# Kernel tuning notes

Hardware: AMD Instinct MI355X
Metric: run time of the kernel (lower is better)

Reference implementation:

```python
import jax, jax.numpy as jnp
import numpy as np

N_NODES = 100000
N_EDGES = 1600000
N_GRAPHS = 128
BEHAVIOR_DIM = 32
LLM_DIM = 768
LLM_PROJ = 32
HIDDEN = 64
NUM_CLASSES = 2
INPUT_DIM = 64 + 16 + LLM_PROJ + BEHAVIOR_DIM  # 144


def gcn_conv(h, edge_index, edge_weight, W, b, n):
    """PyG GCNConv: linear -> gcn_norm with self-loops -> scatter-add at target."""
    h = h @ W  # [N, out]
    row, col = edge_index[0], edge_index[1]
    loop = jnp.arange(n)
    row_f = jnp.concatenate([row, loop])
    col_f = jnp.concatenate([col, loop])
    ew_f = jnp.concatenate([edge_weight, jnp.ones((n,), h.dtype)])
    deg = jax.ops.segment_sum(ew_f, col_f, num_segments=n)
    dinv = jnp.where(deg > 0, jax.lax.rsqrt(deg), 0.0)
    norm = dinv[row_f] * ew_f * dinv[col_f]  # [E+N]
    out = jax.ops.segment_sum(norm[:, None] * h[row_f], col_f, num_segments=n)
    return out + b


def global_mean_pool(x, batch, num_graphs):
    s = jax.ops.segment_sum(x, batch, num_segments=num_graphs)
    cnt = jax.ops.segment_sum(jnp.ones((x.shape[0],), x.dtype), batch, num_segments=num_graphs)
    return s / jnp.maximum(cnt, 1.0)[:, None]


def setup_inputs() -> dict:
    key = jax.random.key(0)
    ks = jax.random.split(key, 16)
    inp = {
        "x_names": jax.random.randint(ks[0], (N_NODES,), 0, 20000),
        "x_types": jax.random.randint(ks[1], (N_NODES,), 0, 100),
        "x_behaviors": jax.random.normal(ks[2], (N_NODES, BEHAVIOR_DIM), jnp.float32),
        "edge_index": jax.random.randint(ks[3], (2, N_EDGES), 0, N_NODES),
        "edge_weight": jax.random.uniform(ks[4], (N_EDGES,), jnp.float32),
        "batch": jnp.sort(jax.random.randint(ks[5], (N_NODES,), 0, N_GRAPHS)),
        "llm_features": jax.random.normal(ks[6], (N_NODES, LLM_DIM), jnp.float32),
        # parameters
        "name_emb": jax.random.normal(ks[7], (20000, 64), jnp.float32),
        "type_emb": jax.random.normal(ks[8], (100, 16), jnp.float32),
        "llm_proj_w": jax.random.normal(ks[9], (LLM_DIM, LLM_PROJ), jnp.float32) * 0.02,
        "llm_proj_b": jnp.zeros((LLM_PROJ,), jnp.float32),
        "conv1_w": jax.random.normal(ks[10], (INPUT_DIM, HIDDEN), jnp.float32) * 0.08,
        "conv1_b": jnp.zeros((HIDDEN,), jnp.float32),
        "conv2_w": jax.random.normal(ks[11], (HIDDEN, HIDDEN), jnp.float32) * 0.12,
        "conv2_b": jnp.zeros((HIDDEN,), jnp.float32),
        "cls_w": jax.random.normal(ks[12], (HIDDEN, NUM_CLASSES), jnp.float32) * 0.12,
        "cls_b": jnp.zeros((NUM_CLASSES,), jnp.float32),
    }
    return inp


def reference(x_names, x_types, x_behaviors, edge_index, edge_weight, batch,
              llm_features, name_emb, type_emb, llm_proj_w, llm_proj_b,
              conv1_w, conv1_b, conv2_w, conv2_b, cls_w, cls_b):
    n = x_names.shape[0]
    name_feat = name_emb[x_names]          # [N, 64]
    type_feat = type_emb[x_types]          # [N, 16]
    llm_feat = llm_features @ llm_proj_w + llm_proj_b  # [N, 32]
    x = jnp.concatenate([name_feat, type_feat, llm_feat, x_behaviors], axis=1)
    # dropout is identity in eval mode
    x = jax.nn.relu(gcn_conv(x, edge_index, edge_weight, conv1_w, conv1_b, n))
    x = jax.nn.relu(gcn_conv(x, edge_index, edge_weight, conv2_w, conv2_b, n))
    x = global_mean_pool(x, batch, N_GRAPHS)  # [G, HIDDEN]
    return x @ cls_w + cls_b                   # [G, 2]
```

## Files before the change

kernel.cpp:

```cpp
#include <hip/hip_runtime.h>
#include <cstdint>
#include <cstddef>

typedef __attribute__((ext_vector_type(8))) _Float16 f16x8;
typedef __attribute__((ext_vector_type(4))) _Float16 f16x4;
typedef __attribute__((ext_vector_type(4))) float f32x4;

__device__ __forceinline__ f16x8 cvt8(const float4& p, const float4& q) {
  f16x8 r;
  r[0] = (_Float16)p.x; r[1] = (_Float16)p.y; r[2] = (_Float16)p.z; r[3] = (_Float16)p.w;
  r[4] = (_Float16)q.x; r[5] = (_Float16)q.y; r[6] = (_Float16)q.z; r[7] = (_Float16)q.w;
  return r;
}


__global__ void prep_kernel(const float* __restrict__ pw, const float* __restrict__ pb,
                            const float* __restrict__ w1, const float* __restrict__ w2,
                            _Float16* __restrict__ Bf, float* __restrict__ biasf,
                            _Float16* __restrict__ B2f, int* __restrict__ cnt, int n) {
  int idx = blockIdx.x * 256 + threadIdx.x;
  if (idx < n) cnt[idx] = 0;
  if (idx < 896 * 64) {
    int gk = idx >> 6, col = idx & 63;
    float val;
    if (gk < 768) {
      float acc = 0.0f;
      #pragma unroll 8
      for (int m = 0; m < 32; ++m) acc = fmaf(pw[gk * 32 + m], w1[(80 + m) * 64 + col], acc);
      val = acc;
    } else if (gk < 832) val = w1[(gk - 768) * 64 + col];
    else if (gk < 848)   val = w1[(64 + gk - 832) * 64 + col];
    else if (gk < 864)   val = w1[(112 + gk - 848) * 64 + col];
    else if (gk < 880)   val = w1[(128 + gk - 864) * 64 + col];
    else                 val = 0.0f;
    int chunk = gk >> 5, k = gk & 31;
    int g, j;
    if (k < 16) { g = k >> 2; j = k & 3; } else { int k2 = k - 16; g = k2 >> 2; j = 4 + (k2 & 3); }
    Bf[((size_t)(chunk * 4 + g) * 64 + col) * 8 + j] = (_Float16)val;
  } else if (idx < 896 * 64 + 64) {
    int col = idx - 896 * 64;
    float acc = 0.0f;
    for (int m = 0; m < 32; ++m) acc = fmaf(pb[m], w1[(80 + m) * 64 + col], acc);
    biasf[col] = acc;
  } else if (idx < 896 * 64 + 64 + 64 * 64) {
    int q2 = idx - (896 * 64 + 64);
    int gk = q2 >> 6, col = q2 & 63;
    float val = w2[gk * 64 + col];
    int chunk = gk >> 5, k = gk & 31;
    int g = k >> 3, j = k & 7;
    B2f[((size_t)(chunk * 4 + g) * 64 + col) * 8 + j] = (_Float16)val;
  }
}


__global__ void cnt_kernel(const int* __restrict__ ei, int* __restrict__ cnt, int E) {
  int e = blockIdx.x * 256 + threadIdx.x;
  if (e < E) atomicAdd(&cnt[ei[E + e]], 1);
}

__global__ __launch_bounds__(256) void scan_blk(const int* __restrict__ cnt,
                                                int* __restrict__ colp,
                                                int* __restrict__ bsum, int n) {
  __shared__ int ws[4];
  int t = threadIdx.x, lane = t & 63, w = t >> 6;
  int i = blockIdx.x * 256 + t;
  int v = (i < n) ? cnt[i] : 0;
  int x = v;
  #pragma unroll
  for (int off = 1; off < 64; off <<= 1) { int y = __shfl_up(x, off); if (lane >= off) x += y; }
  if (lane == 63) ws[w] = x;
  __syncthreads();
  if (t == 0) {
    int s = 0;
    #pragma unroll
    for (int k = 0; k < 4; ++k) { int tmp = ws[k]; ws[k] = s; s += tmp; }
    bsum[blockIdx.x] = s;
  }
  __syncthreads();
  if (i < n) colp[i] = ws[w] + x - v;
}

__global__ __launch_bounds__(512) void scan_top(int* __restrict__ bsum,
                                                int* __restrict__ colp, int nb, int n) {
  __shared__ int ws[8];
  int t = threadIdx.x, lane = t & 63, w = t >> 6;
  int v = (t < nb) ? bsum[t] : 0;
  int x = v;
  #pragma unroll
  for (int off = 1; off < 64; off <<= 1) { int y = __shfl_up(x, off); if (lane >= off) x += y; }
  if (lane == 63) ws[w] = x;
  __syncthreads();
  if (t == 0) {
    int s = 0;
    #pragma unroll
    for (int k = 0; k < 8; ++k) { int tmp = ws[k]; ws[k] = s; s += tmp; }
  }
  __syncthreads();
  int excl = ws[w] + x - v;
  if (t < nb) bsum[t] = excl;
  if (t == nb - 1) colp[n] = excl + v;
}

__global__ void scan_add(int* __restrict__ colp, const int* __restrict__ bsum, int n) {
  int i = blockIdx.x * 256 + threadIdx.x;
  if (i < n) colp[i] += bsum[blockIdx.x];
}

__global__ void fill_kernel(const int* __restrict__ ei, const float* __restrict__ ew,
                            int* __restrict__ colp, int2* __restrict__ csr, int E) {
  int e = blockIdx.x * 256 + threadIdx.x;
  if (e >= E) return;
  int row = ei[e], col = ei[E + e];
  int pos = atomicAdd(&colp[col], 1);
  csr[pos] = make_int2(row, __float_as_int(ew[e]));
}

__global__ void degsum_kernel(const int* __restrict__ colp, const int2* __restrict__ csr,
                              float* __restrict__ dinv, int n) {
  int j = blockIdx.x * 256 + threadIdx.x;
  if (j >= n) return;
  int e0 = (j > 0) ? colp[j - 1] : 0;
  int e1 = colp[j];
  float s = 1.0f;
  for (int e = e0; e < e1; ++e) s += __int_as_float(csr[e].y);
  dinv[j] = rsqrtf(s);
}


__device__ __forceinline__ void loadBf(const _Float16* __restrict__ Bf, int c, int g, int r16,
                                       f16x8 (&bf)[4]) {
  #pragma unroll
  for (int ct = 0; ct < 4; ++ct)
    bf[ct] = *(const f16x8*)(Bf + ((size_t)(c * 4 + g) * 64 + ct * 16 + r16) * 8);
}

__device__ __forceinline__ void mfma8(f32x4 (&acc)[2][4], const f16x8& a0, const f16x8& a1,
                                      const f16x8 (&bf)[4]) {
  #pragma unroll
  for (int ct = 0; ct < 4; ++ct) {
    acc[0][ct] = __builtin_amdgcn_mfma_f32_16x16x32_f16(a0, bf[ct], acc[0][ct], 0, 0, 0);
    acc[1][ct] = __builtin_amdgcn_mfma_f32_16x16x32_f16(a1, bf[ct], acc[1][ct], 0, 0, 0);
  }
}

__global__ __launch_bounds__(256, 3) void gemm1_kernel(
    const float* __restrict__ llm, const _Float16* __restrict__ Bf,
    const int* __restrict__ names, const int* __restrict__ types,
    const float* __restrict__ beh, const float* __restrict__ nemb,
    const float* __restrict__ temb, const float* __restrict__ biasf,
    const float* __restrict__ dinv, _Float16* __restrict__ out, int n)
{
  int nwg = gridDim.x;
  int b = blockIdx.x;
  int q = nwg >> 3, r = nwg & 7;
  int xcd = b & 7, bidx = b >> 3;
  int swz = (xcd < r ? xcd * (q + 1) : r * (q + 1) + (xcd - r) * q) + bidx;

  int w = swz * 4 + (threadIdx.x >> 6);
  int nw = (n + 31) >> 5;
  if (w >= nw) return;
  int lane = threadIdx.x & 63;
  int g = lane >> 4, r16 = lane & 15;
  int base = w * 32;

  int arow0 = base + r16;      if (arow0 > n - 1) arow0 = n - 1;
  int arow1 = base + 16 + r16; if (arow1 > n - 1) arow1 = n - 1;
  int nm0 = names[arow0], nm1 = names[arow1];
  int tp0 = types[arow0], tp1 = types[arow1];

  const float* pA0 = llm + (size_t)arow0 * 768 + g * 4;
  const float* pA1 = llm + (size_t)arow1 * 768 + g * 4;

  f32x4 acc[2][4];
  #pragma unroll
  for (int i = 0; i < 2; ++i)
    #pragma unroll
    for (int j = 0; j < 4; ++j) { acc[i][j][0] = 0.f; acc[i][j][1] = 0.f; acc[i][j][2] = 0.f; acc[i][j][3] = 0.f; }

  float4 X0l = *(const float4*)(pA0 +  0), X0h = *(const float4*)(pA0 + 16);
  float4 X1l = *(const float4*)(pA1 +  0), X1h = *(const float4*)(pA1 + 16);
  float4 Y0l = *(const float4*)(pA0 + 32), Y0h = *(const float4*)(pA0 + 48);
  float4 Y1l = *(const float4*)(pA1 + 32), Y1h = *(const float4*)(pA1 + 48);
  float4 Z0l = *(const float4*)(pA0 + 64), Z0h = *(const float4*)(pA0 + 80);
  float4 Z1l = *(const float4*)(pA1 + 64), Z1h = *(const float4*)(pA1 + 80);

  f16x8 bf[4], a0, a1;

  #pragma unroll 1
  for (int cc = 0; cc < 7; ++cc) {
    const int c = cc * 3;
    loadBf(Bf, c, g, r16, bf);
    a0 = cvt8(X0l, X0h); a1 = cvt8(X1l, X1h);
    X0l = *(const float4*)(pA0 + (c + 3) * 32);
    X0h = *(const float4*)(pA0 + (c + 3) * 32 + 16);
    X1l = *(const float4*)(pA1 + (c + 3) * 32);
    X1h = *(const float4*)(pA1 + (c + 3) * 32 + 16);
    __builtin_amdgcn_sched_barrier(0);
    mfma8(acc, a0, a1, bf);
    loadBf(Bf, c + 1, g, r16, bf);
    a0 = cvt8(Y0l, Y0h); a1 = cvt8(Y1l, Y1h);
    Y0l = *(const float4*)(pA0 + (c + 4) * 32);
    Y0h = *(const float4*)(pA0 + (c + 4) * 32 + 16);
    Y1l = *(const float4*)(pA1 + (c + 4) * 32);
    Y1h = *(const float4*)(pA1 + (c + 4) * 32 + 16);
    __builtin_amdgcn_sched_barrier(0);
    mfma8(acc, a0, a1, bf);
    loadBf(Bf, c + 2, g, r16, bf);
    a0 = cvt8(Z0l, Z0h); a1 = cvt8(Z1l, Z1h);
    Z0l = *(const float4*)(pA0 + (c + 5) * 32);
    Z0h = *(const float4*)(pA0 + (c + 5) * 32 + 16);
    Z1l = *(const float4*)(pA1 + (c + 5) * 32);
    Z1h = *(const float4*)(pA1 + (c + 5) * 32 + 16);
    __builtin_amdgcn_sched_barrier(0);
    mfma8(acc, a0, a1, bf);
  }

  loadBf(Bf, 21, g, r16, bf);
  a0 = cvt8(X0l, X0h); a1 = cvt8(X1l, X1h);
  mfma8(acc, a0, a1, bf);
  loadBf(Bf, 22, g, r16, bf);
  a0 = cvt8(Y0l, Y0h); a1 = cvt8(Y1l, Y1h);
  mfma8(acc, a0, a1, bf);
  loadBf(Bf, 23, g, r16, bf);
  a0 = cvt8(Z0l, Z0h); a1 = cvt8(Z1l, Z1h);
  mfma8(acc, a0, a1, bf);

  const float* pN0 = nemb + (size_t)nm0 * 64 + g * 4;
  const float* pN1 = nemb + (size_t)nm1 * 64 + g * 4;
  #pragma unroll
  for (int t = 0; t < 2; ++t) {
    float4 l0 = *(const float4*)(pN0 + t * 32), h0 = *(const float4*)(pN0 + t * 32 + 16);
    float4 l1 = *(const float4*)(pN1 + t * 32), h1 = *(const float4*)(pN1 + t * 32 + 16);
    loadBf(Bf, 24 + t, g, r16, bf);
    a0 = cvt8(l0, h0); a1 = cvt8(l1, h1);
    mfma8(acc, a0, a1, bf);
  }
  {
    float4 l0 = *(const float4*)(temb + (size_t)tp0 * 16 + g * 4);
    float4 h0 = *(const float4*)(beh + (size_t)arow0 * 32 + g * 4);
    float4 l1 = *(const float4*)(temb + (size_t)tp1 * 16 + g * 4);
    float4 h1 = *(const float4*)(beh + (size_t)arow1 * 32 + g * 4);
    loadBf(Bf, 26, g, r16, bf);
    a0 = cvt8(l0, h0); a1 = cvt8(l1, h1);
    mfma8(acc, a0, a1, bf);
  }
  {
    const float4 z = make_float4(0.f, 0.f, 0.f, 0.f);
    float4 l0 = *(const float4*)(beh + (size_t)arow0 * 32 + 16 + g * 4);
    float4 l1 = *(const float4*)(beh + (size_t)arow1 * 32 + 16 + g * 4);
    loadBf(Bf, 27, g, r16, bf);
    a0 = cvt8(l0, z); a1 = cvt8(l1, z);
    mfma8(acc, a0, a1, bf);
  }

  float dv0[4], dv1[4];
  #pragma unroll
  for (int rr = 0; rr < 4; ++rr) {
    int n0 = base + g * 4 + rr;      dv0[rr] = dinv[n0 < n ? n0 : n - 1];
    int n1 = base + 16 + g * 4 + rr; dv1[rr] = dinv[n1 < n ? n1 : n - 1];
  }
  #pragma unroll
  for (int ct = 0; ct < 4; ++ct) {
    int col = ct * 16 + r16;
    float bfc = biasf[col];
    #pragma unroll
    for (int rr = 0; rr < 4; ++rr) {
      int node0 = base + g * 4 + rr;
      if (node0 < n) out[(size_t)node0 * 64 + col] = (_Float16)((acc[0][ct][rr] + bfc) * dv0[rr]);
      int node1 = base + 16 + g * 4 + rr;
      if (node1 < n) out[(size_t)node1 * 64 + col] = (_Float16)((acc[1][ct][rr] + bfc) * dv1[rr]);
    }
  }
}


__global__ __launch_bounds__(256, 4) void gemm2_kernel(
    const _Float16* __restrict__ h, const _Float16* __restrict__ B2f,
    const float* __restrict__ dinv, _Float16* __restrict__ out, int n)
{
  int w = blockIdx.x * 4 + (threadIdx.x >> 6);
  int nw = (n + 31) >> 5;
  if (w >= nw) return;
  int lane = threadIdx.x & 63;
  int g = lane >> 4, r16 = lane & 15;
  int base = w * 32;
  int arow0 = base + r16;      if (arow0 > n - 1) arow0 = n - 1;
  int arow1 = base + 16 + r16; if (arow1 > n - 1) arow1 = n - 1;

  f32x4 acc[2][4];
  #pragma unroll
  for (int i = 0; i < 2; ++i)
    #pragma unroll
    for (int j = 0; j < 4; ++j) { acc[i][j][0] = 0.f; acc[i][j][1] = 0.f; acc[i][j][2] = 0.f; acc[i][j][3] = 0.f; }

  #pragma unroll
  for (int c = 0; c < 2; ++c) {
    f16x8 bf[4];
    loadBf(B2f, c, g, r16, bf);
    f16x8 a0 = *(const f16x8*)(h + (size_t)arow0 * 64 + c * 32 + g * 8);
    f16x8 a1 = *(const f16x8*)(h + (size_t)arow1 * 64 + c * 32 + g * 8);
    mfma8(acc, a0, a1, bf);
  }

  float dv0[4], dv1[4];
  #pragma unroll
  for (int rr = 0; rr < 4; ++rr) {
    int n0 = base + g * 4 + rr;      dv0[rr] = dinv[n0 < n ? n0 : n - 1];
    int n1 = base + 16 + g * 4 + rr; dv1[rr] = dinv[n1 < n ? n1 : n - 1];
  }
  #pragma unroll
  for (int ct = 0; ct < 4; ++ct) {
    int col = ct * 16 + r16;
    #pragma unroll
    for (int rr = 0; rr < 4; ++rr) {
      int node0 = base + g * 4 + rr;
      if (node0 < n) out[(size_t)node0 * 64 + col] = (_Float16)(acc[0][ct][rr] * dv0[rr]);
      int node1 = base + 16 + g * 4 + rr;
      if (node1 < n) out[(size_t)node1 * 64 + col] = (_Float16)(acc[1][ct][rr] * dv1[rr]);
    }
  }
}


template <typename OUT>
__global__ __launch_bounds__(256) void agg_kernel(
    const _Float16* __restrict__ hp, const int* __restrict__ colp,
    const int2* __restrict__ csr, const float* __restrict__ dinv,
    const float* __restrict__ bias, OUT* __restrict__ out, int n)
{
  int wid = threadIdx.x >> 6, lane = threadIdx.x & 63;
  int j = blockIdx.x * 4 + wid;
  if (j >= n) return;
  float dj = dinv[j];
  float hj = (float)hp[(size_t)j * 64 + lane];
  int e0 = (j > 0) ? colp[j - 1] : 0;
  int e1 = colp[j];
  float s0 = 0.0f, s1 = 0.0f;
  int e = e0;
  for (; e + 8 <= e1; e += 8) {
    int2 m0 = csr[e],     m1 = csr[e + 1], m2 = csr[e + 2], m3 = csr[e + 3];
    int2 m4 = csr[e + 4], m5 = csr[e + 5], m6 = csr[e + 6], m7 = csr[e + 7];
    float f0 = (float)hp[(size_t)m0.x * 64 + lane];
    float f1 = (float)hp[(size_t)m1.x * 64 + lane];
    float f2 = (float)hp[(size_t)m2.x * 64 + lane];
    float f3 = (float)hp[(size_t)m3.x * 64 + lane];
    float f4 = (float)hp[(size_t)m4.x * 64 + lane];
    float f5 = (float)hp[(size_t)m5.x * 64 + lane];
    float f6 = (float)hp[(size_t)m6.x * 64 + lane];
    float f7 = (float)hp[(size_t)m7.x * 64 + lane];
    s0 = fmaf(__int_as_float(m0.y), f0, s0);
    s1 = fmaf(__int_as_float(m1.y), f1, s1);
    s0 = fmaf(__int_as_float(m2.y), f2, s0);
    s1 = fmaf(__int_as_float(m3.y), f3, s1);
    s0 = fmaf(__int_as_float(m4.y), f4, s0);
    s1 = fmaf(__int_as_float(m5.y), f5, s1);
    s0 = fmaf(__int_as_float(m6.y), f6, s0);
    s1 = fmaf(__int_as_float(m7.y), f7, s1);
  }
  for (; e + 2 <= e1; e += 2) {
    int2 m0 = csr[e], m1 = csr[e + 1];
    float f0 = (float)hp[(size_t)m0.x * 64 + lane];
    float f1 = (float)hp[(size_t)m1.x * 64 + lane];
    s0 = fmaf(__int_as_float(m0.y), f0, s0);
    s1 = fmaf(__int_as_float(m1.y), f1, s1);
  }
  if (e < e1) {
    int2 m = csr[e];
    s0 = fmaf(__int_as_float(m.y), (float)hp[(size_t)m.x * 64 + lane], s0);
  }
  float acc = bias[lane] + dj * (hj + s0 + s1);
  out[(size_t)j * 64 + lane] = (OUT)fmaxf(acc, 0.0f);
}


__global__ __launch_bounds__(256) void pool_kernel(const float* __restrict__ x,
                                                   const int* __restrict__ batch,
                                                   float* __restrict__ pooled, int n) {
  __shared__ float red[4][64];
  __shared__ int range_s[2];
  int gph = blockIdx.x;
  int tid = threadIdx.x, wid = tid >> 6, lane = tid & 63;
  if (tid < 2) {
    int target = gph + tid;
    int lo = 0, hi = n;
    while (lo < hi) { int m = (lo + hi) >> 1; if (batch[m] < target) lo = m + 1; else hi = m; }
    range_s[tid] = lo;
  }
  __syncthreads();
  int lo = range_s[0], hi = range_s[1];
  float acc = 0.0f;
  for (int i = lo + wid; i < hi; i += 4) acc += x[(size_t)i * 64 + lane];
  red[wid][lane] = acc;
  __syncthreads();
  if (tid < 64) {
    float sum = red[0][lane] + red[1][lane] + red[2][lane] + red[3][lane];
    float cntf = (float)(hi - lo);
    pooled[gph * 64 + lane] = sum / fmaxf(cntf, 1.0f);
  }
}

__global__ void cls_kernel(const float* __restrict__ pooled, const float* __restrict__ cw,
                           const float* __restrict__ cb, float* __restrict__ out) {
  int t = threadIdx.x;
  int gph = t >> 1, c = t & 1;
  float acc = cb[c];
  #pragma unroll 8
  for (int k = 0; k < 64; ++k) acc = fmaf(pooled[gph * 64 + k], cw[k * 2 + c], acc);
  out[gph * 2 + c] = acc;
}


extern "C" void kernel_launch(void* const* d_in, const int* in_sizes, int n_in,
                              void* d_out, int out_size, void* d_ws, size_t ws_size,
                              hipStream_t stream) {
  const int*   x_names  = (const int*)  d_in[0];
  const int*   x_types  = (const int*)  d_in[1];
  const float* behav    = (const float*)d_in[2];
  const int*   ei       = (const int*)  d_in[3];
  const float* ew       = (const float*)d_in[4];
  const int*   batch    = (const int*)  d_in[5];
  const float* llm      = (const float*)d_in[6];
  const float* name_emb = (const float*)d_in[7];
  const float* type_emb = (const float*)d_in[8];
  const float* pw       = (const float*)d_in[9];
  const float* pb       = (const float*)d_in[10];
  const float* w1       = (const float*)d_in[11];
  const float* b1       = (const float*)d_in[12];
  const float* w2       = (const float*)d_in[13];
  const float* b2       = (const float*)d_in[14];
  const float* cw       = (const float*)d_in[15];
  const float* cb       = (const float*)d_in[16];

  const int N = in_sizes[0];
  const int E = in_sizes[4];
  const int nb = (N + 255) / 256;
  const int eb = (E + 255) / 256;
  const int gblocks = ((N + 31) / 32 + 3) / 4;

  char* p = (char*)d_ws;
  auto alloc = [&](size_t bytes) -> void* {
    void* r = (void*)p; p += (bytes + 255) & ~(size_t)255; return r;
  };
  float*     dinv   = (float*)    alloc((size_t)N * 4);
  int*       cnt    = (int*)      alloc((size_t)N * 4);
  int*       colp   = (int*)      alloc((size_t)(N + 1) * 4);
  int2*      csr    = (int2*)     alloc((size_t)E * 8);
  int*       bsum   = (int*)      alloc((size_t)(nb + 1) * 4);
  _Float16*  Bf     = (_Float16*) alloc((size_t)896 * 64 * 2);
  _Float16*  B2f    = (_Float16*) alloc((size_t)64 * 64 * 2);
  float*     biasf  = (float*)    alloc((size_t)64 * 4);
  _Float16*  hp1    = (_Float16*) alloc((size_t)N * 64 * 2);
  _Float16*  y1     = (_Float16*) alloc((size_t)N * 64 * 2);
  _Float16*  hp2    = (_Float16*) alloc((size_t)N * 64 * 2);
  float*     y2     = (float*)    alloc((size_t)N * 64 * 4);
  float*     pooled = (float*)    alloc((size_t)128 * 64 * 4);
  (void)ws_size; (void)n_in; (void)out_size;

  int prep_blocks = (896 * 64 + 64 + 64 * 64 + 255) / 256;
  if (prep_blocks < nb) prep_blocks = nb;
  prep_kernel<<<prep_blocks, 256, 0, stream>>>(pw, pb, w1, w2, Bf, biasf, B2f, cnt, N);
  cnt_kernel<<<eb, 256, 0, stream>>>(ei, cnt, E);
  scan_blk<<<nb, 256, 0, stream>>>(cnt, colp, bsum, N);
  scan_top<<<1, 512, 0, stream>>>(bsum, colp, nb, N);
  scan_add<<<nb, 256, 0, stream>>>(colp, bsum, N);
  fill_kernel<<<eb, 256, 0, stream>>>(ei, ew, colp, csr, E);
  degsum_kernel<<<nb, 256, 0, stream>>>(colp, csr, dinv, N);

  gemm1_kernel<<<gblocks, 256, 0, stream>>>(llm, Bf, x_names, x_types, behav,
                                            name_emb, type_emb, biasf, dinv, hp1, N);
  agg_kernel<_Float16><<<(N + 3) / 4, 256, 0, stream>>>(hp1, colp, csr, dinv, b1, y1, N);
  gemm2_kernel<<<gblocks, 256, 0, stream>>>(y1, B2f, dinv, hp2, N);
  agg_kernel<float><<<(N + 3) / 4, 256, 0, stream>>>(hp2, colp, csr, dinv, b2, y2, N);
  pool_kernel<<<128, 256, 0, stream>>>(y2, batch, pooled, N);
  cls_kernel<<<1, 256, 0, stream>>>(pooled, cw, cb, (float*)d_out);
}
```

Baseline: 490.2 us.

## Stage LLM rows in LDS for gemm1 and split output columns across waves

gemm1 now has each 256-thread block load a 32-row tile of the fp32 LLM features with fully coalesced float4 loads, convert it to fp16 into shared memory, and then let four waves share it. Each wave computes 16 rows by 32 columns. Before, each wave streamed its own 32 rows with strided per-lane loads. The B-fragment layout in prep is changed to a simple k>>3 / k&7 packing to match the new A fragment order, and the tail embedding gathers are reworked to match. This is meant to improve global load coalescing and shrink register use, at the cost of about 50KB of LDS per block, a barrier, and less overlap of loads with MFMA.

```diff
diff --git a/kernel.cpp b/kernel.cpp
--- a/kernel.cpp
+++ b/kernel.cpp
@@ -30,12 +30,10 @@
       val = acc;
     } else if (gk < 832) val = w1[(gk - 768) * 64 + col];
     else if (gk < 848)   val = w1[(64 + gk - 832) * 64 + col];
-    else if (gk < 864)   val = w1[(112 + gk - 848) * 64 + col];
-    else if (gk < 880)   val = w1[(128 + gk - 864) * 64 + col];
+    else if (gk < 880)   val = w1[(112 + gk - 848) * 64 + col];
     else                 val = 0.0f;
     int chunk = gk >> 5, k = gk & 31;
-    int g, j;
-    if (k < 16) { g = k >> 2; j = k & 3; } else { int k2 = k - 16; g = k2 >> 2; j = 4 + (k2 & 3); }
+    int g = k >> 3, j = k & 7;
     Bf[((size_t)(chunk * 4 + g) * 64 + col) * 8 + j] = (_Float16)val;
   } else if (idx < 896 * 64 + 64) {
     int col = idx - 896 * 64;
@@ -127,21 +125,8 @@
 }
 
 
-__device__ __forceinline__ void loadBf(const _Float16* __restrict__ Bf, int c, int g, int r16,
-                                       f16x8 (&bf)[4]) {
-  #pragma unroll
-  for (int ct = 0; ct < 4; ++ct)
-    bf[ct] = *(const f16x8*)(Bf + ((size_t)(c * 4 + g) * 64 + ct * 16 + r16) * 8);
-}
-
-__device__ __forceinline__ void mfma8(f32x4 (&acc)[2][4], const f16x8& a0, const f16x8& a1,
-                                      const f16x8 (&bf)[4]) {
-  #pragma unroll
-  for (int ct = 0; ct < 4; ++ct) {
-    acc[0][ct] = __builtin_amdgcn_mfma_f32_16x16x32_f16(a0, bf[ct], acc[0][ct], 0, 0, 0);
-    acc[1][ct] = __builtin_amdgcn_mfma_f32_16x16x32_f16(a1, bf[ct], acc[1][ct], 0, 0, 0);
-  }
-}
+#define G1_ROWS 32
+#define G1_STR  776
 
 __global__ __launch_bounds__(256, 3) void gemm1_kernel(
     const float* __restrict__ llm, const _Float16* __restrict__ Bf,
@@ -150,129 +135,121 @@
     const float* __restrict__ temb, const float* __restrict__ biasf,
     const float* __restrict__ dinv, _Float16* __restrict__ out, int n)
 {
+  __shared__ _Float16 As[G1_ROWS][G1_STR];
+
   int nwg = gridDim.x;
   int b = blockIdx.x;
   int q = nwg >> 3, r = nwg & 7;
   int xcd = b & 7, bidx = b >> 3;
   int swz = (xcd < r ? xcd * (q + 1) : r * (q + 1) + (xcd - r) * q) + bidx;
 
-  int w = swz * 4 + (threadIdx.x >> 6);
-  int nw = (n + 31) >> 5;
-  if (w >= nw) return;
-  int lane = threadIdx.x & 63;
-  int g = lane >> 4, r16 = lane & 15;
-  int base = w * 32;
-
-  int arow0 = base + r16;      if (arow0 > n - 1) arow0 = n - 1;
-  int arow1 = base + 16 + r16; if (arow1 > n - 1) arow1 = n - 1;
-  int nm0 = names[arow0], nm1 = names[arow1];
-  int tp0 = types[arow0], tp1 = types[arow1];
-
-  const float* pA0 = llm + (size_t)arow0 * 768 + g * 4;
-  const float* pA1 = llm + (size_t)arow1 * 768 + g * 4;
-
-  f32x4 acc[2][4];
-  #pragma unroll
-  for (int i = 0; i < 2; ++i)
-    #pragma unroll
-    for (int j = 0; j < 4; ++j) { acc[i][j][0] = 0.f; acc[i][j][1] = 0.f; acc[i][j][2] = 0.f; acc[i][j][3] = 0.f; }
-
-  float4 X0l = *(const float4*)(pA0 +  0), X0h = *(const float4*)(pA0 + 16);
-  float4 X1l = *(const float4*)(pA1 +  0), X1h = *(const float4*)(pA1 + 16);
-  float4 Y0l = *(const float4*)(pA0 + 32), Y0h = *(const float4*)(pA0 + 48);
-  float4 Y1l = *(const float4*)(pA1 + 32), Y1h = *(const float4*)(pA1 + 48);
-  float4 Z0l = *(const float4*)(pA0 + 64), Z0h = *(const float4*)(pA0 + 80);
-  float4 Z1l = *(const float4*)(pA1 + 64), Z1h = *(const float4*)(pA1 + 80);
-
-  f16x8 bf[4], a0, a1;
-
-  #pragma unroll 1
-  for (int cc = 0; cc < 7; ++cc) {
-    const int c = cc * 3;
-    loadBf(Bf, c, g, r16, bf);
-    a0 = cvt8(X0l, X0h); a1 = cvt8(X1l, X1h);
-    X0l = *(const float4*)(pA0 + (c + 3) * 32);
-    X0h = *(const float4*)(pA0 + (c + 3) * 32 + 16);
-    X1l = *(const float4*)(pA1 + (c + 3) * 32);
-    X1h = *(const float4*)(pA1 + (c + 3) * 32 + 16);
-    __builtin_amdgcn_sched_barrier(0);
-    mfma8(acc, a0, a1, bf);
-    loadBf(Bf, c + 1, g, r16, bf);
-    a0 = cvt8(Y0l, Y0h); a1 = cvt8(Y1l, Y1h);
-    Y0l = *(const float4*)(pA0 + (c + 4) * 32);
-    Y0h = *(const float4*)(pA0 + (c + 4) * 32 + 16);
-    Y1l = *(const float4*)(pA1 + (c + 4) * 32);
-    Y1h = *(const float4*)(pA1 + (c + 4) * 32 + 16);
-    __builtin_amdgcn_sched_barrier(0);
-    mfma8(acc, a0, a1, bf);
-    loadBf(Bf, c + 2, g, r16, bf);
-    a0 = cvt8(Z0l, Z0h); a1 = cvt8(Z1l, Z1h);
-    Z0l = *(const float4*)(pA0 + (c + 5) * 32);
-    Z0h = *(const float4*)(pA0 + (c + 5) * 32 + 16);
-    Z1l = *(const float4*)(pA1 + (c + 5) * 32);
-    Z1h = *(const float4*)(pA1 + (c + 5) * 32 + 16);
-    __builtin_amdgcn_sched_barrier(0);
-    mfma8(acc, a0, a1, bf);
-  }
-
-  loadBf(Bf, 21, g, r16, bf);
-  a0 = cvt8(X0l, X0h); a1 = cvt8(X1l, X1h);
-  mfma8(acc, a0, a1, bf);
-  loadBf(Bf, 22, g, r16, bf);
-  a0 = cvt8(Y0l, Y0h); a1 = cvt8(Y1l, Y1h);
-  mfma8(acc, a0, a1, bf);
-  loadBf(Bf, 23, g, r16, bf);
-  a0 = cvt8(Z0l, Z0h); a1 = cvt8(Z1l, Z1h);
-  mfma8(acc, a0, a1, bf);
-
-  const float* pN0 = nemb + (size_t)nm0 * 64 + g * 4;
-  const float* pN1 = nemb + (size_t)nm1 * 64 + g * 4;
-  #pragma unroll
-  for (int t = 0; t < 2; ++t) {
-    float4 l0 = *(const float4*)(pN0 + t * 32), h0 = *(const float4*)(pN0 + t * 32 + 16);
-    float4 l1 = *(const float4*)(pN1 + t * 32), h1 = *(const float4*)(pN1 + t * 32 + 16);
-    loadBf(Bf, 24 + t, g, r16, bf);
-    a0 = cvt8(l0, h0); a1 = cvt8(l1, h1);
-    mfma8(acc, a0, a1, bf);
-  }
+  const int tid = threadIdx.x;
+  const int base = swz * G1_ROWS;
+
+  const float* srcbase = llm + (size_t)base * 768;
+  bool safe = (base + G1_ROWS <= n);
+  #pragma unroll
+  for (int i = 0; i < 24; ++i) {
+    int f = i * 1024 + tid * 4;
+    int row = f / 768;
+    int k = f - row * 768;
+    const float* sp;
+    if (safe) sp = srcbase + f;
+    else {
+      int grow = base + row; if (grow > n - 1) grow = n - 1;
+      sp = llm + (size_t)grow * 768 + k;
+    }
+    float4 v = *(const float4*)sp;
+    f16x4 h;
+    h[0] = (_Float16)v.x; h[1] = (_Float16)v.y;
+    h[2] = (_Float16)v.z; h[3] = (_Float16)v.w;
+    *(f16x4*)&As[row][k] = h;
+  }
+  __syncthreads();
+
+  const int lane = tid & 63, wv = tid >> 6;
+  const int g = lane >> 4, r16 = lane & 15;
+  const int rowHalf = (wv & 1) * 16;
+  const int cbase = (wv >> 1) * 2;
+
+  int arowG = base + rowHalf + r16; if (arowG > n - 1) arowG = n - 1;
+  int nm = names[arowG], tp = types[arowG];
+
+  f32x4 acc0, acc1;
+  acc0[0] = 0.f; acc0[1] = 0.f; acc0[2] = 0.f; acc0[3] = 0.f;
+  acc1 = acc0;
+
+  #pragma unroll 4
+  for (int c = 0; c < 24; ++c) {
+    f16x8 b0 = *(const f16x8*)(Bf + ((size_t)(c * 4 + g) * 64 + cbase * 16 + r16) * 8);
+    f16x8 b1 = *(const f16x8*)(Bf + ((size_t)(c * 4 + g) * 64 + (cbase + 1) * 16 + r16) * 8);
+    f16x8 a = *(const f16x8*)&As[rowHalf + r16][c * 32 + g * 8];
+    acc0 = __builtin_amdgcn_mfma_f32_16x16x32_f16(a, b0, acc0, 0, 0, 0);
+    acc1 = __builtin_amdgcn_mfma_f32_16x16x32_f16(a, b1, acc1, 0, 0, 0);
+  }
+
+  auto tailStep = [&](int c, const float4& p, const float4& qv) {
+    f16x8 b0 = *(const f16x8*)(Bf + ((size_t)(c * 4 + g) * 64 + cbase * 16 + r16) * 8);
+    f16x8 b1 = *(const f16x8*)(Bf + ((size_t)(c * 4 + g) * 64 + (cbase + 1) * 16 + r16) * 8);
+    f16x8 a = cvt8(p, qv);
+    acc0 = __builtin_amdgcn_mfma_f32_16x16x32_f16(a, b0, acc0, 0, 0, 0);
+    acc1 = __builtin_amdgcn_mfma_f32_16x16x32_f16(a, b1, acc1, 0, 0, 0);
+  };
+
   {
-    float4 l0 = *(const float4*)(temb + (size_t)tp0 * 16 + g * 4);
-    float4 h0 = *(const float4*)(beh + (size_t)arow0 * 32 + g * 4);
-    float4 l1 = *(const float4*)(temb + (size_t)tp1 * 16 + g * 4);
-    float4 h1 = *(const float4*)(beh + (size_t)arow1 * 32 + g * 4);
-    loadBf(Bf, 26, g, r16, bf);
-    a0 = cvt8(l0, h0); a1 = cvt8(l1, h1);
-    mfma8(acc, a0, a1, bf);
+    const float* pN = nemb + (size_t)nm * 64 + g * 8;
+    tailStep(24, *(const float4*)pN, *(const float4*)(pN + 4));
+    tailStep(25, *(const float4*)(pN + 32), *(const float4*)(pN + 36));
+  }
+  {
+    const float* q0 = (g < 2) ? (temb + (size_t)tp * 16 + g * 8)
+                              : (beh + (size_t)arowG * 32 + (size_t)(g - 2) * 8);
+    tailStep(26, *(const float4*)q0, *(const float4*)(q0 + 4));
   }
   {
     const float4 z = make_float4(0.f, 0.f, 0.f, 0.f);
-    float4 l0 = *(const float4*)(beh + (size_t)arow0 * 32 + 16 + g * 4);
-    float4 l1 = *(const float4*)(beh + (size_t)arow1 * 32 + 16 + g * 4);
-    loadBf(Bf, 27, g, r16, bf);
-    a0 = cvt8(l0, z); a1 = cvt8(l1, z);
-    mfma8(acc, a0, a1, bf);
-  }
-
-  float dv0[4], dv1[4];
+    const float* q1 = beh + (size_t)arowG * 32 + 16 + (size_t)(g & 1) * 8;
+    float4 p = *(const float4*)q1, qv = *(const float4*)(q1 + 4);
+    if (g >= 2) { p = z; qv = z; }
+    tailStep(27, p, qv);
+  }
+
+  int nodeBase = base + rowHalf + g * 4;
+  float dv[4];
   #pragma unroll
   for (int rr = 0; rr < 4; ++rr) {
-    int n0 = base + g * 4 + rr;      dv0[rr] = dinv[n0 < n ? n0 : n - 1];
-    int n1 = base + 16 + g * 4 + rr; dv1[rr] = dinv[n1 < n ? n1 : n - 1];
-  }
-  #pragma unroll
-  for (int ct = 0; ct < 4; ++ct) {
-    int col = ct * 16 + r16;
+    int nd = nodeBase + rr;
+    dv[rr] = dinv[nd < n ? nd : n - 1];
+  }
+  #pragma unroll
+  for (int ct2 = 0; ct2 < 2; ++ct2) {
+    int col = (cbase + ct2) * 16 + r16;
     float bfc = biasf[col];
+    f32x4 av = (ct2 == 0) ? acc0 : acc1;
     #pragma unroll
     for (int rr = 0; rr < 4; ++rr) {
-      int node0 = base + g * 4 + rr;
-      if (node0 < n) out[(size_t)node0 * 64 + col] = (_Float16)((acc[0][ct][rr] + bfc) * dv0[rr]);
-      int node1 = base + 16 + g * 4 + rr;
-      if (node1 < n) out[(size_t)node1 * 64 + col] = (_Float16)((acc[1][ct][rr] + bfc) * dv1[rr]);
+      int nd = nodeBase + rr;
+      if (nd < n) out[(size_t)nd * 64 + col] = (_Float16)((av[rr] + bfc) * dv[rr]);
     }
   }
 }
 
+
+__device__ __forceinline__ void loadBf(const _Float16* __restrict__ Bf, int c, int g, int r16,
+                                       f16x8 (&bf)[4]) {
+  #pragma unroll
+  for (int ct = 0; ct < 4; ++ct)
+    bf[ct] = *(const f16x8*)(Bf + ((size_t)(c * 4 + g) * 64 + ct * 16 + r16) * 8);
+}
+
+__device__ __forceinline__ void mfma8(f32x4 (&acc)[2][4], const f16x8& a0, const f16x8& a1,
+                                      const f16x8 (&bf)[4]) {
+  #pragma unroll
+  for (int ct = 0; ct < 4; ++ct) {
+    acc[0][ct] = __builtin_amdgcn_mfma_f32_16x16x32_f16(a0, bf[ct], acc[0][ct], 0, 0, 0);
+    acc[1][ct] = __builtin_amdgcn_mfma_f32_16x16x32_f16(a1, bf[ct], acc[1][ct], 0, 0, 0);
+  }
+}
 
 __global__ __launch_bounds__(256, 4) void gemm2_kernel(
     const _Float16* __restrict__ h, const _Float16* __restrict__ B2f,
@@ -321,6 +298,9 @@
   }
 }
 
+
+__device__ __forceinline__ void storeOut(_Float16* p, float v) { *p = (_Float16)v; }
+__device__ __forceinline__ void storeOut(float* p, float v) { *p = v; }
 
 template <typename OUT>
 __global__ __launch_bounds__(256) void agg_kernel(
@@ -369,7 +349,7 @@
     s0 = fmaf(__int_as_float(m.y), (float)hp[(size_t)m.x * 64 + lane], s0);
   }
   float acc = bias[lane] + dj * (hj + s0 + s1);
-  out[(size_t)j * 64 + lane] = (OUT)fmaxf(acc, 0.0f);
+  storeOut(out + (size_t)j * 64 + lane, fmaxf(acc, 0.0f));
 }
 
 
@@ -435,7 +415,8 @@
   const int E = in_sizes[4];
   const int nb = (N + 255) / 256;
   const int eb = (E + 255) / 256;
-  const int gblocks = ((N + 31) / 32 + 3) / 4;
+  const int g1blocks = (N + G1_ROWS - 1) / G1_ROWS;
+  const int g2blocks = ((N + 31) / 32 + 3) / 4;
 
   char* p = (char*)d_ws;
   auto alloc = [&](size_t bytes) -> void* {
@@ -466,10 +447,10 @@
   fill_kernel<<<eb, 256, 0, stream>>>(ei, ew, colp, csr, E);
   degsum_kernel<<<nb, 256, 0, stream>>>(colp, csr, dinv, N);
 
-  gemm1_kernel<<<gblocks, 256, 0, stream>>>(llm, Bf, x_names, x_types, behav,
-                                            name_emb, type_emb, biasf, dinv, hp1, N);
+  gemm1_kernel<<<g1blocks, 256, 0, stream>>>(llm, Bf, x_names, x_types, behav,
+                                             name_emb, type_emb, biasf, dinv, hp1, N);
   agg_kernel<_Float16><<<(N + 3) / 4, 256, 0, stream>>>(hp1, colp, csr, dinv, b1, y1, N);
-  gemm2_kernel<<<gblocks, 256, 0, stream>>>(y1, B2f, dinv, hp2, N);
+  gemm2_kernel<<<g2blocks, 256, 0, stream>>>(y1, B2f, dinv, hp2, N);
   agg_kernel<float><<<(N + 3) / 4, 256, 0, stream>>>(hp2, colp, csr, dinv, b2, y2, N);
   pool_kernel<<<128, 256, 0, stream>>>(y2, batch, pooled, N);
   cls_kernel<<<1, 256, 0, stream>>>(pooled, cw, cb, (float*)d_out);
```

Result: slower. 511.5 us (+4.4%).

## Deepen gemm1 A-prefetch to six chunks with contiguous 8-float K lanes

Applied to the files above, without the earlier changes.

The packed B layout for the first GEMM is changed so that each lane group holds 8 consecutive K values. The llm, embedding and behavior loads now read two adjacent float4s (32 contiguous bytes per lane) instead of two float4s 16 floats apart. The prefetch pipeline grows from three to six in-flight K chunks, which hides more global-load latency but needs more registers at the same launch bounds. The type/behavior tail chunks are remapped to match the new layout, and the agg store is routed through an overloaded helper.

```diff
diff --git a/kernel.cpp b/kernel.cpp
--- a/kernel.cpp
+++ b/kernel.cpp
@@ -30,12 +30,10 @@
       val = acc;
     } else if (gk < 832) val = w1[(gk - 768) * 64 + col];
     else if (gk < 848)   val = w1[(64 + gk - 832) * 64 + col];
-    else if (gk < 864)   val = w1[(112 + gk - 848) * 64 + col];
-    else if (gk < 880)   val = w1[(128 + gk - 864) * 64 + col];
+    else if (gk < 880)   val = w1[(112 + gk - 848) * 64 + col];
     else                 val = 0.0f;
     int chunk = gk >> 5, k = gk & 31;
-    int g, j;
-    if (k < 16) { g = k >> 2; j = k & 3; } else { int k2 = k - 16; g = k2 >> 2; j = 4 + (k2 & 3); }
+    int g = k >> 3, j = k & 7;
     Bf[((size_t)(chunk * 4 + g) * 64 + col) * 8 + j] = (_Float16)val;
   } else if (idx < 896 * 64 + 64) {
     int col = idx - 896 * 64;
@@ -143,6 +141,24 @@
   }
 }
 
+#define LOADSLOT(s, c) \
+  s##0 = *(const float4*)(pA0 + (c) * 32); \
+  s##1 = *(const float4*)(pA0 + (c) * 32 + 4); \
+  s##2 = *(const float4*)(pA1 + (c) * 32); \
+  s##3 = *(const float4*)(pA1 + (c) * 32 + 4);
+
+#define STEPPF(s, c, pc) \
+  loadBf(Bf, (c), g, r16, bf); \
+  a0 = cvt8(s##0, s##1); a1 = cvt8(s##2, s##3); \
+  LOADSLOT(s, pc) \
+  __builtin_amdgcn_sched_barrier(0); \
+  mfma8(acc, a0, a1, bf);
+
+#define STEPNP(s, c) \
+  loadBf(Bf, (c), g, r16, bf); \
+  a0 = cvt8(s##0, s##1); a1 = cvt8(s##2, s##3); \
+  mfma8(acc, a0, a1, bf);
+
 __global__ __launch_bounds__(256, 3) void gemm1_kernel(
     const float* __restrict__ llm, const _Float16* __restrict__ Bf,
     const int* __restrict__ names, const int* __restrict__ types,
@@ -165,91 +181,78 @@
 
   int arow0 = base + r16;      if (arow0 > n - 1) arow0 = n - 1;
   int arow1 = base + 16 + r16; if (arow1 > n - 1) arow1 = n - 1;
+
+  const float* pA0 = llm + (size_t)arow0 * 768 + g * 8;
+  const float* pA1 = llm + (size_t)arow1 * 768 + g * 8;
+
+  float4 Pa0, Pa1, Pa2, Pa3, Pb0, Pb1, Pb2, Pb3, Pc0, Pc1, Pc2, Pc3;
+  float4 Pd0, Pd1, Pd2, Pd3, Pe0, Pe1, Pe2, Pe3, Pf0, Pf1, Pf2, Pf3;
+  LOADSLOT(Pa, 0)
+  LOADSLOT(Pb, 1)
+  LOADSLOT(Pc, 2)
+  LOADSLOT(Pd, 3)
+  LOADSLOT(Pe, 4)
+  LOADSLOT(Pf, 5)
+
   int nm0 = names[arow0], nm1 = names[arow1];
   int tp0 = types[arow0], tp1 = types[arow1];
 
-  const float* pA0 = llm + (size_t)arow0 * 768 + g * 4;
-  const float* pA1 = llm + (size_t)arow1 * 768 + g * 4;
-
   f32x4 acc[2][4];
   #pragma unroll
   for (int i = 0; i < 2; ++i)
     #pragma unroll
     for (int j = 0; j < 4; ++j) { acc[i][j][0] = 0.f; acc[i][j][1] = 0.f; acc[i][j][2] = 0.f; acc[i][j][3] = 0.f; }
 
-  float4 X0l = *(const float4*)(pA0 +  0), X0h = *(const float4*)(pA0 + 16);
-  float4 X1l = *(const float4*)(pA1 +  0), X1h = *(const float4*)(pA1 + 16);
-  float4 Y0l = *(const float4*)(pA0 + 32), Y0h = *(const float4*)(pA0 + 48);
-  float4 Y1l = *(const float4*)(pA1 + 32), Y1h = *(const float4*)(pA1 + 48);
-  float4 Z0l = *(const float4*)(pA0 + 64), Z0h = *(const float4*)(pA0 + 80);
-  float4 Z1l = *(const float4*)(pA1 + 64), Z1h = *(const float4*)(pA1 + 80);
-
   f16x8 bf[4], a0, a1;
 
   #pragma unroll 1
-  for (int cc = 0; cc < 7; ++cc) {
-    const int c = cc * 3;
-    loadBf(Bf, c, g, r16, bf);
-    a0 = cvt8(X0l, X0h); a1 = cvt8(X1l, X1h);
-    X0l = *(const float4*)(pA0 + (c + 3) * 32);
-    X0h = *(const float4*)(pA0 + (c + 3) * 32 + 16);
-    X1l = *(const float4*)(pA1 + (c + 3) * 32);
-    X1h = *(const float4*)(pA1 + (c + 3) * 32 + 16);
-    __builtin_amdgcn_sched_barrier(0);
-    mfma8(acc, a0, a1, bf);
-    loadBf(Bf, c + 1, g, r16, bf);
-    a0 = cvt8(Y0l, Y0h); a1 = cvt8(Y1l, Y1h);
-    Y0l = *(const float4*)(pA0 + (c + 4) * 32);
-    Y0h = *(const float4*)(pA0 + (c + 4) * 32 + 16);
-    Y1l = *(const float4*)(pA1 + (c + 4) * 32);
-    Y1h = *(const float4*)(pA1 + (c + 4) * 32 + 16);
-    __builtin_amdgcn_sched_barrier(0);
-    mfma8(acc, a0, a1, bf);
-    loadBf(Bf, c + 2, g, r16, bf);
-    a0 = cvt8(Z0l, Z0h); a1 = cvt8(Z1l, Z1h);
-    Z0l = *(const float4*)(pA0 + (c + 5) * 32);
-    Z0h = *(const float4*)(pA0 + (c + 5) * 32 + 16);
-    Z1l = *(const float4*)(pA1 + (c + 5) * 32);
-    Z1h = *(const float4*)(pA1 + (c + 5) * 32 + 16);
-    __builtin_amdgcn_sched_barrier(0);
-    mfma8(acc, a0, a1, bf);
-  }
-
-  loadBf(Bf, 21, g, r16, bf);
-  a0 = cvt8(X0l, X0h); a1 = cvt8(X1l, X1h);
-  mfma8(acc, a0, a1, bf);
-  loadBf(Bf, 22, g, r16, bf);
-  a0 = cvt8(Y0l, Y0h); a1 = cvt8(Y1l, Y1h);
-  mfma8(acc, a0, a1, bf);
-  loadBf(Bf, 23, g, r16, bf);
-  a0 = cvt8(Z0l, Z0h); a1 = cvt8(Z1l, Z1h);
-  mfma8(acc, a0, a1, bf);
-
-  const float* pN0 = nemb + (size_t)nm0 * 64 + g * 4;
-  const float* pN1 = nemb + (size_t)nm1 * 64 + g * 4;
+  for (int cc = 0; cc < 3; ++cc) {
+    const int c = cc * 6;
+    STEPPF(Pa, c + 0, c + 6)
+    STEPPF(Pb, c + 1, c + 7)
+    STEPPF(Pc, c + 2, c + 8)
+    STEPPF(Pd, c + 3, c + 9)
+    STEPPF(Pe, c + 4, c + 10)
+    STEPPF(Pf, c + 5, c + 11)
+  }
+
+  STEPNP(Pa, 18)
+  STEPNP(Pb, 19)
+  STEPNP(Pc, 20)
+  STEPNP(Pd, 21)
+  STEPNP(Pe, 22)
+  STEPNP(Pf, 23)
+
+  const float* pN0 = nemb + (size_t)nm0 * 64 + g * 8;
+  const float* pN1 = nemb + (size_t)nm1 * 64 + g * 8;
   #pragma unroll
   for (int t = 0; t < 2; ++t) {
-    float4 l0 = *(const float4*)(pN0 + t * 32), h0 = *(const float4*)(pN0 + t * 32 + 16);
-    float4 l1 = *(const float4*)(pN1 + t * 32), h1 = *(const float4*)(pN1 + t * 32 + 16);
+    float4 l0 = *(const float4*)(pN0 + t * 32), h0 = *(const float4*)(pN0 + t * 32 + 4);
+    float4 l1 = *(const float4*)(pN1 + t * 32), h1 = *(const float4*)(pN1 + t * 32 + 4);
     loadBf(Bf, 24 + t, g, r16, bf);
     a0 = cvt8(l0, h0); a1 = cvt8(l1, h1);
     mfma8(acc, a0, a1, bf);
   }
   {
-    float4 l0 = *(const float4*)(temb + (size_t)tp0 * 16 + g * 4);
-    float4 h0 = *(const float4*)(beh + (size_t)arow0 * 32 + g * 4);
-    float4 l1 = *(const float4*)(temb + (size_t)tp1 * 16 + g * 4);
-    float4 h1 = *(const float4*)(beh + (size_t)arow1 * 32 + g * 4);
+    const float* q0 = (g < 2) ? (temb + (size_t)tp0 * 16 + g * 8)
+                              : (beh + (size_t)arow0 * 32 + (size_t)(g - 2) * 8);
+    const float* q1 = (g < 2) ? (temb + (size_t)tp1 * 16 + g * 8)
+                              : (beh + (size_t)arow1 * 32 + (size_t)(g - 2) * 8);
+    float4 l0 = *(const float4*)q0, h0 = *(const float4*)(q0 + 4);
+    float4 l1 = *(const float4*)q1, h1 = *(const float4*)(q1 + 4);
     loadBf(Bf, 26, g, r16, bf);
     a0 = cvt8(l0, h0); a1 = cvt8(l1, h1);
     mfma8(acc, a0, a1, bf);
   }
   {
     const float4 z = make_float4(0.f, 0.f, 0.f, 0.f);
-    float4 l0 = *(const float4*)(beh + (size_t)arow0 * 32 + 16 + g * 4);
-    float4 l1 = *(const float4*)(beh + (size_t)arow1 * 32 + 16 + g * 4);
+    const float* r0 = beh + (size_t)arow0 * 32 + 16 + (size_t)(g & 1) * 8;
+    const float* r1 = beh + (size_t)arow1 * 32 + 16 + (size_t)(g & 1) * 8;
+    float4 l0 = *(const float4*)r0, h0 = *(const float4*)(r0 + 4);
+    float4 l1 = *(const float4*)r1, h1 = *(const float4*)(r1 + 4);
+    if (g >= 2) { l0 = z; h0 = z; l1 = z; h1 = z; }
     loadBf(Bf, 27, g, r16, bf);
-    a0 = cvt8(l0, z); a1 = cvt8(l1, z);
+    a0 = cvt8(l0, h0); a1 = cvt8(l1, h1);
     mfma8(acc, a0, a1, bf);
   }
 
@@ -272,6 +275,10 @@
     }
   }
 }
+
+#undef LOADSLOT
+#undef STEPPF
+#undef STEPNP
 
 
 __global__ __launch_bounds__(256, 4) void gemm2_kernel(
@@ -321,6 +328,9 @@
   }
 }
 
+
+__device__ __forceinline__ void storeOut(_Float16* p, float v) { *p = (_Float16)v; }
+__device__ __forceinline__ void storeOut(float* p, float v) { *p = v; }
 
 template <typename OUT>
 __global__ __launch_bounds__(256) void agg_kernel(
@@ -369,7 +379,7 @@
     s0 = fmaf(__int_as_float(m.y), (float)hp[(size_t)m.x * 64 + lane], s0);
   }
   float acc = bias[lane] + dj * (hj + s0 + s1);
-  out[(size_t)j * 64 + lane] = (OUT)fmaxf(acc, 0.0f);
+  storeOut(out + (size_t)j * 64 + lane, fmaxf(acc, 0.0f));
 }
 
 
```

New measurement: 673.3 us. 1.37x slower.
